# Optimization experiments

Measured on AMD Instinct MI355X. Metric: run time of the kernel, lower is better.

Reference implementation:

```python
import jax, jax.numpy as jnp
import numpy as np

N_NODES = 100000
N_EDGES = 500000
IN_DIM = 128
OUT_DIM = 128
NUM_HEADS = 4
HEAD_DIM = OUT_DIM // NUM_HEADS  # 32


def setup_inputs() -> dict:
    key = jax.random.key(0)
    k1, k2, k3, k4, k5, k6 = jax.random.split(key, 6)
    features = jax.random.normal(k1, (N_NODES, IN_DIM), dtype=jnp.float32)
    edge_index = jax.random.randint(k2, (2, N_EDGES), 0, N_NODES, dtype=jnp.int64)
    W_lin = jax.random.normal(k3, (OUT_DIM, IN_DIM), dtype=jnp.float32) * 0.05
    b_lin = jax.random.normal(k4, (OUT_DIM,), dtype=jnp.float32) * 0.05
    W_att = jax.random.normal(k5, (NUM_HEADS, 2 * OUT_DIM), dtype=jnp.float32) * 0.05
    b_att = jax.random.normal(k6, (NUM_HEADS,), dtype=jnp.float32) * 0.05
    return {"features": features, "edge_index": edge_index,
            "W_lin": W_lin, "b_lin": b_lin, "W_att": W_att, "b_att": b_att}


def reference(features, edge_index, W_lin, b_lin, W_att, b_att):
    num_nodes = features.shape[0]
    h = features @ W_lin.T + b_lin                     # [N, D]
    src, dst = edge_index[0], edge_index[1]
    src_h = h[src]                                     # [E, D]
    dst_h = h[dst]                                     # [E, D]
    # attention = Linear(cat([src_h, dst_h])) without materializing the concat
    logits = src_h @ W_att[:, :OUT_DIM].T + dst_h @ W_att[:, OUT_DIM:].T + b_att  # [E, H]
    # original softmaxes over dim=0 (all edges), per head
    attn = jax.nn.softmax(logits, axis=0)              # [E, H]
    # FAITHFUL quirk: only the first head_dim columns of src_h feed every head
    msgs = src_h[:, None, :HEAD_DIM] * attn[:, :, None]  # [E, H, head_dim]
    agg = jax.ops.segment_sum(msgs.reshape(msgs.shape[0], -1), dst,
                              num_segments=num_nodes)  # [N, H*head_dim] head-major
    return agg + h                                     # dropout(p=0) is identity
```

## Files before the change

### kernel.cpp

```cpp
#include <hip/hip_runtime.h>
#include <hip/hip_bf16.h>
#include <stdint.h>

#define N_NODES  100000
#define N_EDGES  500000
#define DIM      128
#define NUM_HEADS 4
#define HEAD_DIM  32
#define CAP      28

#define C_BLOCKS ((N_EDGES + 255) / 256)
#define G_BLOCKS (N_NODES / 32)

typedef __attribute__((ext_vector_type(8))) __bf16 bf16x8;
typedef __attribute__((ext_vector_type(4))) __bf16 bf16x4;
typedef __attribute__((ext_vector_type(4))) float  f32x4;

__device__ __forceinline__ bf16x8 cvt8(const float* __restrict__ p)
{
    const float4 lo = *reinterpret_cast<const float4*>(p);
    const float4 hi = *reinterpret_cast<const float4*>(p + 4);
    bf16x8 r;
    r[0] = (__bf16)lo.x; r[1] = (__bf16)lo.y; r[2] = (__bf16)lo.z; r[3] = (__bf16)lo.w;
    r[4] = (__bf16)hi.x; r[5] = (__bf16)hi.y; r[6] = (__bf16)hi.z; r[7] = (__bf16)hi.w;
    return r;
}

__device__ __forceinline__ bf16x8 cvt8r(const float4 lo, const float4 hi)
{
    bf16x8 r;
    r[0] = (__bf16)lo.x; r[1] = (__bf16)lo.y; r[2] = (__bf16)lo.z; r[3] = (__bf16)lo.w;
    r[4] = (__bf16)hi.x; r[5] = (__bf16)hi.y; r[6] = (__bf16)hi.z; r[7] = (__bf16)hi.w;
    return r;
}

__device__ __forceinline__ unsigned pack2_bf16(float a, float b)
{
    const __bf16 ba = (__bf16)a, bb = (__bf16)b;
    const unsigned short ua = __builtin_bit_cast(unsigned short, ba);
    const unsigned short ub = __builtin_bit_cast(unsigned short, bb);
    return (unsigned)ua | ((unsigned)ub << 16);
}

__device__ __forceinline__ float unpack_bf16(unsigned p, int hi)
{
    const unsigned short u = (unsigned short)(hi ? (p >> 16) : p);
    const __bf16 b = __builtin_bit_cast(__bf16, u);
    return (float)b;
}

__global__ __launch_bounds__(256) void cvt_wlin_kernel(
    const float* __restrict__ Wlin,
    __bf16* __restrict__ wb)
{
    const int t    = blockIdx.x * 256 + threadIdx.x;
    const int jt   = t >> 8;
    const int kc   = (t >> 6) & 3;
    const int quad = (t >> 4) & 3;
    const int m    = t & 15;
    const bf16x8 o = cvt8(Wlin + (size_t)(jt * 16 + m) * DIM + kc * 32 + quad * 8);
    *reinterpret_cast<bf16x8*>(wb + (size_t)t * 8) = o;
}

__global__ __launch_bounds__(256) void gemm_dots_kernel(
    const float* __restrict__ feat,
    const __bf16* __restrict__ wb,
    const float* __restrict__ blin,
    const float* __restrict__ Watt,
    float* __restrict__ h,
    __bf16* __restrict__ h32,
    float* __restrict__ a_src,
    float* __restrict__ a_dst)
{
    __shared__ float wl[1280];
    __shared__ float bl_l[128];
    __shared__ float sm[2][2][16][8];
    const int tid = threadIdx.x;

    const int wv   = tid >> 6;
    const int g    = wv >> 1;
    const int ch   = wv & 1;
    const int lane = tid & 63;
    const int m    = lane & 15;
    const int quad = lane >> 4;
    const int node0 = (blockIdx.x * 2 + g) * 16;
    const int node  = node0 + m;

    float wstage[4];
#pragma unroll
    for (int i = 0; i < 4; ++i) wstage[i] = Watt[tid + i * 256];
    float blv = 0.f;
    if (tid < 128) blv = blin[tid];

    const float* __restrict__ arow = feat + (size_t)node * DIM + quad * 8;
    float4 alo[4], ahi[4];
#pragma unroll
    for (int kc = 0; kc < 4; ++kc) {
        alo[kc] = *reinterpret_cast<const float4*>(arow + kc * 32);
        ahi[kc] = *reinterpret_cast<const float4*>(arow + kc * 32 + 4);
    }

#pragma unroll
    for (int i = 0; i < 4; ++i) {
        const int t  = tid + i * 256;
        const int hd = t >> 8;
        const int cf = t & 255;
        const int c  = cf & 127;
        const int df = cf >> 7;
        wl[c * 10 + df * 4 + hd] = wstage[i];
    }
    if (tid < 128) bl_l[tid] = blv;
    __syncthreads();

    f32x4 acc[4];
#pragma unroll
    for (int jtl = 0; jtl < 4; ++jtl) acc[jtl] = (f32x4){0.f, 0.f, 0.f, 0.f};

    const bf16x8* __restrict__ wf =
        reinterpret_cast<const bf16x8*>(wb) + (size_t)ch * 16 * 64 + lane;

#pragma unroll
    for (int kc = 0; kc < 4; ++kc) {
        const bf16x8 a = cvt8r(alo[kc], ahi[kc]);
        bf16x8 b[4];
#pragma unroll
        for (int jtl = 0; jtl < 4; ++jtl) b[jtl] = wf[(jtl * 4 + kc) * 64];
#pragma unroll
        for (int jtl = 0; jtl < 4; ++jtl)
            acc[jtl] = __builtin_amdgcn_mfma_f32_16x16x32_bf16(b[jtl], a, acc[jtl], 0, 0, 0);
    }

    float dsrc[4] = {0.f, 0.f, 0.f, 0.f};
    float ddst[4] = {0.f, 0.f, 0.f, 0.f};

#pragma unroll
    for (int jtl = 0; jtl < 4; ++jtl) {
        const int jtg  = ch * 4 + jtl;
        const int col0 = jtg * 16 + quad * 4;
        const float4 bl4 = *reinterpret_cast<const float4*>(&bl_l[col0]);
        float w[40];
#pragma unroll
        for (int k = 0; k < 10; ++k)
            *reinterpret_cast<float4*>(&w[k * 4]) =
                *reinterpret_cast<const float4*>(&wl[col0 * 10 + k * 4]);

        float hv[4];
        hv[0] = acc[jtl][0] + bl4.x;
        hv[1] = acc[jtl][1] + bl4.y;
        hv[2] = acc[jtl][2] + bl4.z;
        hv[3] = acc[jtl][3] + bl4.w;

        const float4 st = {hv[0], hv[1], hv[2], hv[3]};
        *reinterpret_cast<float4*>(h + (size_t)node * DIM + col0) = st;
        if (jtg < 2) {
            bf16x4 o;
            o[0] = (__bf16)hv[0]; o[1] = (__bf16)hv[1];
            o[2] = (__bf16)hv[2]; o[3] = (__bf16)hv[3];
            *reinterpret_cast<bf16x4*>(h32 + (size_t)node * HEAD_DIM + col0) = o;
        }
#pragma unroll
        for (int r = 0; r < 4; ++r) {
#pragma unroll
            for (int hd = 0; hd < 4; ++hd) {
                dsrc[hd] += hv[r] * w[r * 10 + hd];
                ddst[hd] += hv[r] * w[r * 10 + 4 + hd];
            }
        }
    }

#pragma unroll
    for (int off = 16; off <= 32; off <<= 1) {
#pragma unroll
        for (int i = 0; i < 4; ++i) {
            dsrc[i] += __shfl_xor(dsrc[i], off, 64);
            ddst[i] += __shfl_xor(ddst[i], off, 64);
        }
    }
    if (quad == 0) {
#pragma unroll
        for (int i = 0; i < 4; ++i) {
            sm[g][ch][m][i]     = dsrc[i];
            sm[g][ch][m][4 + i] = ddst[i];
        }
    }
    __syncthreads();
    if (ch == 0 && quad == 0) {
        const float4 s = {dsrc[0] + sm[g][1][m][0], dsrc[1] + sm[g][1][m][1],
                          dsrc[2] + sm[g][1][m][2], dsrc[3] + sm[g][1][m][3]};
        const float4 d = {ddst[0] + sm[g][1][m][4], ddst[1] + sm[g][1][m][5],
                          ddst[2] + sm[g][1][m][6], ddst[3] + sm[g][1][m][7]};
        *reinterpret_cast<float4*>(a_src + (size_t)node * 4) = s;
        *reinterpret_cast<float4*>(a_dst + (size_t)node * 4) = d;
    }
}

__global__ __launch_bounds__(256) void edge_exp_bucket_kernel(
    const int* __restrict__ ei,
    const float* __restrict__ a_src,
    const float* __restrict__ a_dst,
    const float* __restrict__ batt,
    float* __restrict__ partials,
    int* __restrict__ cursor,
    int4* __restrict__ slots)
{
    __shared__ float lds[4][4];
    const int e = blockIdx.x * 256 + threadIdx.x;
    const int wv = threadIdx.x >> 6;
    const int lane = threadIdx.x & 63;
    float ex0 = 0.f, ex1 = 0.f, ex2 = 0.f, ex3 = 0.f;
    if (e < N_EDGES) {
        const int s = ei[e];
        const int d = ei[N_EDGES + e];
        const float4 as = *reinterpret_cast<const float4*>(a_src + (size_t)s * 4);
        const float4 ad = *reinterpret_cast<const float4*>(a_dst + (size_t)d * 4);
        ex0 = __expf(as.x + ad.x + batt[0]);
        ex1 = __expf(as.y + ad.y + batt[1]);
        ex2 = __expf(as.z + ad.z + batt[2]);
        ex3 = __expf(as.w + ad.w + batt[3]);
        const int pos = atomicAdd(&cursor[d], 1);
        if (pos < CAP) {
            int4 q;
            q.x = s;
            q.y = (int)pack2_bf16(ex0, ex1);
            q.z = (int)pack2_bf16(ex2, ex3);
            q.w = 0;
            slots[(size_t)d * CAP + pos] = q;
        }
    }
#pragma unroll
    for (int off = 32; off > 0; off >>= 1) {
        ex0 += __shfl_xor(ex0, off, 64);
        ex1 += __shfl_xor(ex1, off, 64);
        ex2 += __shfl_xor(ex2, off, 64);
        ex3 += __shfl_xor(ex3, off, 64);
    }
    if (lane == 0) {
        lds[wv][0] = ex0; lds[wv][1] = ex1; lds[wv][2] = ex2; lds[wv][3] = ex3;
    }
    __syncthreads();
    if (threadIdx.x < 4) {
        const float s = lds[0][threadIdx.x] + lds[1][threadIdx.x]
                      + lds[2][threadIdx.x] + lds[3][threadIdx.x];
        atomicAdd(&partials[(blockIdx.x & 7) * 4 + threadIdx.x], s);
    }
}

__global__ __launch_bounds__(256) void aggregate_kernel(
    const float* __restrict__ h,
    const __bf16* __restrict__ h32,
    const float* __restrict__ partials,
    const int* __restrict__ cursor,
    const int4* __restrict__ slots,
    float* __restrict__ out)
{
    const int nv = blockIdx.x * 4 + (threadIdx.x >> 6);
    const int lane = threadIdx.x & 63;
    if (nv >= N_NODES) return;
    const int n = __builtin_amdgcn_readfirstlane(nv);

    const int hd0 = lane >> 5;
    const int dd  = lane & 31;

    const float hn0 = h[(size_t)n * DIM + lane];
    const float hn1 = h[(size_t)n * DIM + 64 + lane];
    const int cnt_raw = cursor[n];

    const float4* __restrict__ p4 = reinterpret_cast<const float4*>(partials);
    float Sx = 0.f, Sy = 0.f, Sz = 0.f, Sw = 0.f;
#pragma unroll
    for (int b = 0; b < 8; ++b) {
        const float4 t = p4[b];
        Sx += t.x; Sy += t.y; Sz += t.z; Sw += t.w;
    }
    const float inv0 = 1.0f / (hd0 ? Sy : Sx);
    const float inv1 = 1.0f / (hd0 ? Sw : Sz);

    const int cnt = cnt_raw > CAP ? CAP : cnt_raw;
    const int4* __restrict__ sl = slots + (size_t)n * CAP;

    float acc0 = 0.f, acc1 = 0.f;
    int j = 0;
    for (; j + 4 <= cnt; j += 4) {
        const int4 q0 = sl[j];
        const int4 q1 = sl[j + 1];
        const int4 q2 = sl[j + 2];
        const int4 q3 = sl[j + 3];
        const float v0 = (float)h32[(size_t)q0.x * HEAD_DIM + dd];
        const float v1 = (float)h32[(size_t)q1.x * HEAD_DIM + dd];
        const float v2 = (float)h32[(size_t)q2.x * HEAD_DIM + dd];
        const float v3 = (float)h32[(size_t)q3.x * HEAD_DIM + dd];
        acc0 += v0 * unpack_bf16((unsigned)q0.y, hd0);
        acc1 += v0 * unpack_bf16((unsigned)q0.z, hd0);
        acc0 += v1 * unpack_bf16((unsigned)q1.y, hd0);
        acc1 += v1 * unpack_bf16((unsigned)q1.z, hd0);
        acc0 += v2 * unpack_bf16((unsigned)q2.y, hd0);
        acc1 += v2 * unpack_bf16((unsigned)q2.z, hd0);
        acc0 += v3 * unpack_bf16((unsigned)q3.y, hd0);
        acc1 += v3 * unpack_bf16((unsigned)q3.z, hd0);
    }
    for (; j < cnt; ++j) {
        const int4 q = sl[j];
        const float v = (float)h32[(size_t)q.x * HEAD_DIM + dd];
        acc0 += v * unpack_bf16((unsigned)q.y, hd0);
        acc1 += v * unpack_bf16((unsigned)q.z, hd0);
    }
    out[(size_t)n * DIM + lane]      = acc0 * inv0 + hn0;
    out[(size_t)n * DIM + 64 + lane] = acc1 * inv1 + hn1;
}

extern "C" void kernel_launch(void* const* d_in, const int* in_sizes, int n_in,
                              void* d_out, int out_size, void* d_ws, size_t ws_size,
                              hipStream_t stream)
{
    const float* feat = (const float*)d_in[0];
    const int*   ei   = (const int*)d_in[1];
    const float* Wlin = (const float*)d_in[2];
    const float* blin = (const float*)d_in[3];
    const float* Watt = (const float*)d_in[4];
    const float* batt = (const float*)d_in[5];
    float*       out  = (float*)d_out;

    const size_t NF = (size_t)N_NODES * DIM;
    float*  h        = (float*)d_ws;
    float*  a_src    = h + NF;
    float*  a_dst    = a_src + (size_t)N_NODES * 4;
    int*    cursor   = (int*)(a_dst + (size_t)N_NODES * 4);
    float*  partials = (float*)(cursor + N_NODES);
    int4*   slots    = (int4*)(partials + 32);
    __bf16* h32      = (__bf16*)(slots + (size_t)N_NODES * CAP);
    __bf16* wlin_bf  = h32 + (size_t)N_NODES * HEAD_DIM;

    hipMemsetAsync(cursor, 0, (size_t)N_NODES * sizeof(int) + 32 * sizeof(float), stream);

    cvt_wlin_kernel<<<8, 256, 0, stream>>>(Wlin, wlin_bf);
    gemm_dots_kernel<<<G_BLOCKS, 256, 0, stream>>>(feat, wlin_bf, blin, Watt,
                                                   h, h32, a_src, a_dst);
    edge_exp_bucket_kernel<<<C_BLOCKS, 256, 0, stream>>>(ei, a_src, a_dst, batt,
                                                         partials, cursor, slots);
    aggregate_kernel<<<25000, 256, 0, stream>>>(h, h32, partials, cursor, slots, out);
}
```

Baseline: 194.9 us.

## Store only source ids in buckets and recompute edge exponentials during aggregation

The edge kernel now writes a 4-byte source index per bucket slot instead of a 16-byte record with packed bf16 exponentials, and each thread handles two edges using vectorised int2 index loads. The aggregate kernel recomputes exp(a_src + a_dst + b) per edge from a gathered a_src float4 and a per-node a_dst. This cuts slot write and read traffic and drops the bf16 rounding of the attention weights. In exchange it adds a random 16-byte a_src gather and extra exp calls per lane in the aggregation loop.

```diff
diff --git a/kernel.cpp b/kernel.cpp
--- a/kernel.cpp
+++ b/kernel.cpp
@@ -9,7 +9,7 @@
 #define HEAD_DIM  32
 #define CAP      28
 
-#define C_BLOCKS ((N_EDGES + 255) / 256)
+#define E_BLOCKS ((N_EDGES / 2 + 255) / 256)
 #define G_BLOCKS (N_NODES / 32)
 
 typedef __attribute__((ext_vector_type(8))) __bf16 bf16x8;
@@ -32,21 +32,6 @@
     r[0] = (__bf16)lo.x; r[1] = (__bf16)lo.y; r[2] = (__bf16)lo.z; r[3] = (__bf16)lo.w;
     r[4] = (__bf16)hi.x; r[5] = (__bf16)hi.y; r[6] = (__bf16)hi.z; r[7] = (__bf16)hi.w;
     return r;
-}
-
-__device__ __forceinline__ unsigned pack2_bf16(float a, float b)
-{
-    const __bf16 ba = (__bf16)a, bb = (__bf16)b;
-    const unsigned short ua = __builtin_bit_cast(unsigned short, ba);
-    const unsigned short ub = __builtin_bit_cast(unsigned short, bb);
-    return (unsigned)ua | ((unsigned)ub << 16);
-}
-
-__device__ __forceinline__ float unpack_bf16(unsigned p, int hi)
-{
-    const unsigned short u = (unsigned short)(hi ? (p >> 16) : p);
-    const __bf16 b = __builtin_bit_cast(__bf16, u);
-    return (float)b;
 }
 
 __global__ __launch_bounds__(256) void cvt_wlin_kernel(
@@ -201,30 +186,37 @@
     const float* __restrict__ batt,
     float* __restrict__ partials,
     int* __restrict__ cursor,
-    int4* __restrict__ slots)
+    int* __restrict__ slot_src)
 {
     __shared__ float lds[4][4];
-    const int e = blockIdx.x * 256 + threadIdx.x;
+    const int t = blockIdx.x * 256 + threadIdx.x;
     const int wv = threadIdx.x >> 6;
     const int lane = threadIdx.x & 63;
+    const int e0 = t * 2;
     float ex0 = 0.f, ex1 = 0.f, ex2 = 0.f, ex3 = 0.f;
-    if (e < N_EDGES) {
-        const int s = ei[e];
-        const int d = ei[N_EDGES + e];
-        const float4 as = *reinterpret_cast<const float4*>(a_src + (size_t)s * 4);
-        const float4 ad = *reinterpret_cast<const float4*>(a_dst + (size_t)d * 4);
-        ex0 = __expf(as.x + ad.x + batt[0]);
-        ex1 = __expf(as.y + ad.y + batt[1]);
-        ex2 = __expf(as.z + ad.z + batt[2]);
-        ex3 = __expf(as.w + ad.w + batt[3]);
-        const int pos = atomicAdd(&cursor[d], 1);
-        if (pos < CAP) {
-            int4 q;
-            q.x = s;
-            q.y = (int)pack2_bf16(ex0, ex1);
-            q.z = (int)pack2_bf16(ex2, ex3);
-            q.w = 0;
-            slots[(size_t)d * CAP + pos] = q;
+    if (e0 < N_EDGES) {
+        const int2 ss = *reinterpret_cast<const int2*>(ei + e0);
+        const int2 dd = *reinterpret_cast<const int2*>(ei + N_EDGES + e0);
+        const float b0 = batt[0], b1 = batt[1], b2 = batt[2], b3 = batt[3];
+        {
+            const float4 as = *reinterpret_cast<const float4*>(a_src + (size_t)ss.x * 4);
+            const float4 ad = *reinterpret_cast<const float4*>(a_dst + (size_t)dd.x * 4);
+            ex0 += __expf(as.x + ad.x + b0);
+            ex1 += __expf(as.y + ad.y + b1);
+            ex2 += __expf(as.z + ad.z + b2);
+            ex3 += __expf(as.w + ad.w + b3);
+            const int pos = atomicAdd(&cursor[dd.x], 1);
+            if (pos < CAP) slot_src[(size_t)dd.x * CAP + pos] = ss.x;
+        }
+        {
+            const float4 as = *reinterpret_cast<const float4*>(a_src + (size_t)ss.y * 4);
+            const float4 ad = *reinterpret_cast<const float4*>(a_dst + (size_t)dd.y * 4);
+            ex0 += __expf(as.x + ad.x + b0);
+            ex1 += __expf(as.y + ad.y + b1);
+            ex2 += __expf(as.z + ad.z + b2);
+            ex3 += __expf(as.w + ad.w + b3);
+            const int pos = atomicAdd(&cursor[dd.y], 1);
+            if (pos < CAP) slot_src[(size_t)dd.y * CAP + pos] = ss.y;
         }
     }
 #pragma unroll
@@ -248,9 +240,12 @@
 __global__ __launch_bounds__(256) void aggregate_kernel(
     const float* __restrict__ h,
     const __bf16* __restrict__ h32,
+    const float* __restrict__ a_src,
+    const float* __restrict__ a_dst,
+    const float* __restrict__ batt,
     const float* __restrict__ partials,
     const int* __restrict__ cursor,
-    const int4* __restrict__ slots,
+    const int* __restrict__ slot_src,
     float* __restrict__ out)
 {
     const int nv = blockIdx.x * 4 + (threadIdx.x >> 6);
@@ -264,6 +259,10 @@
     const float hn0 = h[(size_t)n * DIM + lane];
     const float hn1 = h[(size_t)n * DIM + 64 + lane];
     const int cnt_raw = cursor[n];
+    const float4 ad4 = *reinterpret_cast<const float4*>(a_dst + (size_t)n * 4);
+
+    const float bd0 = (hd0 ? ad4.y : ad4.x) + (hd0 ? batt[1] : batt[0]);
+    const float bd1 = (hd0 ? ad4.w : ad4.z) + (hd0 ? batt[3] : batt[2]);
 
     const float4* __restrict__ p4 = reinterpret_cast<const float4*>(partials);
     float Sx = 0.f, Sy = 0.f, Sz = 0.f, Sw = 0.f;
@@ -276,33 +275,35 @@
     const float inv1 = 1.0f / (hd0 ? Sw : Sz);
 
     const int cnt = cnt_raw > CAP ? CAP : cnt_raw;
-    const int4* __restrict__ sl = slots + (size_t)n * CAP;
+    const int* __restrict__ sl = slot_src + (size_t)n * CAP;
 
     float acc0 = 0.f, acc1 = 0.f;
     int j = 0;
     for (; j + 4 <= cnt; j += 4) {
-        const int4 q0 = sl[j];
-        const int4 q1 = sl[j + 1];
-        const int4 q2 = sl[j + 2];
-        const int4 q3 = sl[j + 3];
-        const float v0 = (float)h32[(size_t)q0.x * HEAD_DIM + dd];
-        const float v1 = (float)h32[(size_t)q1.x * HEAD_DIM + dd];
-        const float v2 = (float)h32[(size_t)q2.x * HEAD_DIM + dd];
-        const float v3 = (float)h32[(size_t)q3.x * HEAD_DIM + dd];
-        acc0 += v0 * unpack_bf16((unsigned)q0.y, hd0);
-        acc1 += v0 * unpack_bf16((unsigned)q0.z, hd0);
-        acc0 += v1 * unpack_bf16((unsigned)q1.y, hd0);
-        acc1 += v1 * unpack_bf16((unsigned)q1.z, hd0);
-        acc0 += v2 * unpack_bf16((unsigned)q2.y, hd0);
-        acc1 += v2 * unpack_bf16((unsigned)q2.z, hd0);
-        acc0 += v3 * unpack_bf16((unsigned)q3.y, hd0);
-        acc1 += v3 * unpack_bf16((unsigned)q3.z, hd0);
+        const int s0 = sl[j], s1 = sl[j + 1], s2 = sl[j + 2], s3 = sl[j + 3];
+        const float4 A0 = *reinterpret_cast<const float4*>(a_src + (size_t)s0 * 4);
+        const float4 A1 = *reinterpret_cast<const float4*>(a_src + (size_t)s1 * 4);
+        const float4 A2 = *reinterpret_cast<const float4*>(a_src + (size_t)s2 * 4);
+        const float4 A3 = *reinterpret_cast<const float4*>(a_src + (size_t)s3 * 4);
+        const float v0 = (float)h32[(size_t)s0 * HEAD_DIM + dd];
+        const float v1 = (float)h32[(size_t)s1 * HEAD_DIM + dd];
+        const float v2 = (float)h32[(size_t)s2 * HEAD_DIM + dd];
+        const float v3 = (float)h32[(size_t)s3 * HEAD_DIM + dd];
+        acc0 += v0 * __expf((hd0 ? A0.y : A0.x) + bd0);
+        acc1 += v0 * __expf((hd0 ? A0.w : A0.z) + bd1);
+        acc0 += v1 * __expf((hd0 ? A1.y : A1.x) + bd0);
+        acc1 += v1 * __expf((hd0 ? A1.w : A1.z) + bd1);
+        acc0 += v2 * __expf((hd0 ? A2.y : A2.x) + bd0);
+        acc1 += v2 * __expf((hd0 ? A2.w : A2.z) + bd1);
+        acc0 += v3 * __expf((hd0 ? A3.y : A3.x) + bd0);
+        acc1 += v3 * __expf((hd0 ? A3.w : A3.z) + bd1);
     }
     for (; j < cnt; ++j) {
-        const int4 q = sl[j];
-        const float v = (float)h32[(size_t)q.x * HEAD_DIM + dd];
-        acc0 += v * unpack_bf16((unsigned)q.y, hd0);
-        acc1 += v * unpack_bf16((unsigned)q.z, hd0);
+        const int s = sl[j];
+        const float4 A = *reinterpret_cast<const float4*>(a_src + (size_t)s * 4);
+        const float v = (float)h32[(size_t)s * HEAD_DIM + dd];
+        acc0 += v * __expf((hd0 ? A.y : A.x) + bd0);
+        acc1 += v * __expf((hd0 ? A.w : A.z) + bd1);
     }
     out[(size_t)n * DIM + lane]      = acc0 * inv0 + hn0;
     out[(size_t)n * DIM + 64 + lane] = acc1 * inv1 + hn1;
@@ -326,8 +327,8 @@
     float*  a_dst    = a_src + (size_t)N_NODES * 4;
     int*    cursor   = (int*)(a_dst + (size_t)N_NODES * 4);
     float*  partials = (float*)(cursor + N_NODES);
-    int4*   slots    = (int4*)(partials + 32);
-    __bf16* h32      = (__bf16*)(slots + (size_t)N_NODES * CAP);
+    int*    slot_src = (int*)(partials + 32);
+    __bf16* h32      = (__bf16*)(slot_src + (size_t)N_NODES * CAP);
     __bf16* wlin_bf  = h32 + (size_t)N_NODES * HEAD_DIM;
 
     hipMemsetAsync(cursor, 0, (size_t)N_NODES * sizeof(int) + 32 * sizeof(float), stream);
@@ -335,7 +336,8 @@
     cvt_wlin_kernel<<<8, 256, 0, stream>>>(Wlin, wlin_bf);
     gemm_dots_kernel<<<G_BLOCKS, 256, 0, stream>>>(feat, wlin_bf, blin, Watt,
                                                    h, h32, a_src, a_dst);
-    edge_exp_bucket_kernel<<<C_BLOCKS, 256, 0, stream>>>(ei, a_src, a_dst, batt,
-                                                         partials, cursor, slots);
-    aggregate_kernel<<<25000, 256, 0, stream>>>(h, h32, partials, cursor, slots, out);
-}
+    edge_exp_bucket_kernel<<<E_BLOCKS, 256, 0, stream>>>(ei, a_src, a_dst, batt,
+                                                         partials, cursor, slot_src);
+    aggregate_kernel<<<25000, 256, 0, stream>>>(h, h32, a_src, a_dst, batt,
+                                                partials, cursor, slot_src, out);
+}
```

Result: no change. 197.4 us (+1.3%).
